# Kernel optimization log

Hardware: AMD Instinct MI355X
Metric: run time of the kernel (lower is better)

## Reference

```python
import jax, jax.numpy as jnp
import numpy as np

B, S, D, H = 4, 2048, 1024, 16
DK = D // H


def setup_inputs() -> dict:
    key = jax.random.key(0)
    k1, k2, k3, k4 = jax.random.split(key, 4)
    x = jax.random.normal(k1, (B, S, D), dtype=jnp.float32)
    # torch nn.Linear stores weight as [out, in]; y = x @ W.T + b
    w_qkv = jax.random.normal(k2, (3 * D, D), dtype=jnp.float32) * (1.0 / np.sqrt(D))
    b_qkv = jax.random.normal(k3, (3 * D,), dtype=jnp.float32) * 0.02
    w_o = jax.random.normal(k4, (D, D), dtype=jnp.float32) * (1.0 / np.sqrt(D))
    # causal mask: True where attention is disallowed (masked_fill semantics)
    mask = jnp.triu(jnp.ones((S, S), dtype=bool), k=1)[None, None]  # [1,1,S,S]
    return {"encodings_for_qkv": x, "mask": mask, "w_qkv": w_qkv, "b_qkv": b_qkv, "w_o": w_o}


def reference(encodings_for_qkv, mask, w_qkv, b_qkv, w_o):
    x = encodings_for_qkv
    qkv = x @ w_qkv.T + b_qkv                      # [B,S,3D]
    q, k, v = jnp.split(qkv, 3, axis=-1)           # each [B,S,D]

    def heads(t):
        return t.reshape(B, S, H, DK).transpose(0, 2, 1, 3)  # [B,H,S,DK]

    q, k, v = heads(q), heads(k), heads(v)
    scale = 1.0 / np.sqrt(DK).astype(np.float32)
    sims = jnp.einsum('bhqd,bhkd->bhqk', q, k) * scale       # [B,H,S,S]
    sims = jnp.where(mask, jnp.float32(-1e9), sims)
    attn = jax.nn.softmax(sims, axis=-1)
    out = jnp.einsum('bhqk,bhkd->bhqd', attn, v)             # [B,H,S,DK]
    out = out.transpose(0, 2, 1, 3).reshape(B, S, D)
    return out @ w_o.T
```

## Files before the change

### kernel.cpp

```cpp
#include <hip/hip_runtime.h>
#include <hip/hip_bf16.h>

typedef __attribute__((ext_vector_type(8))) __bf16 bf16x8;
typedef __attribute__((ext_vector_type(4))) __bf16 bf16x4;
typedef __attribute__((ext_vector_type(4))) float f32x4;

constexpr int B = 4, S = 2048, D = 1024, H = 16, DK = 64;

#define GLOAD16(gp, lp)                                                              \
  __builtin_amdgcn_global_load_lds((const __attribute__((address_space(1))) void*)(gp), \
                                   (__attribute__((address_space(3))) void*)(lp), 16, 0, 0)

__global__ __launch_bounds__(256) void convert_bf16(const float* __restrict__ X,
                                                    const float* __restrict__ Wqkv,
                                                    const float* __restrict__ Wo,
                                                    __bf16* __restrict__ Xb,
                                                    __bf16* __restrict__ Wqkvb,
                                                    __bf16* __restrict__ Wob) {
  const int NX = B * S * D;
  const int NW = 3 * D * D;
  const int NO = D * D;
  const int total8 = (NX + NW + NO) / 8;
  for (int i = blockIdx.x * blockDim.x + threadIdx.x; i < total8;
       i += gridDim.x * blockDim.x) {
    const int e = i * 8;
    const float* src;
    __bf16* dst;
    int off;
    if (e < NX) {
      src = X; dst = Xb; off = e;
    } else if (e < NX + NW) {
      src = Wqkv; dst = Wqkvb; off = e - NX;
    } else {
      src = Wo; dst = Wob; off = e - NX - NW;
    }
    float4 a = *reinterpret_cast<const float4*>(src + off);
    float4 b = *reinterpret_cast<const float4*>(src + off + 4);
    bf16x8 v = {(__bf16)a.x, (__bf16)a.y, (__bf16)a.z, (__bf16)a.w,
                (__bf16)b.x, (__bf16)b.y, (__bf16)b.z, (__bf16)b.w};
    *reinterpret_cast<bf16x8*>(dst + off) = v;
  }
}

__global__ __launch_bounds__(256) void qkv_gemm(const __bf16* __restrict__ Xb,
                                                const __bf16* __restrict__ Wb,
                                                const float* __restrict__ bias,
                                                __bf16* __restrict__ Qb,
                                                __bf16* __restrict__ Kb,
                                                __bf16* __restrict__ VTb) {
  __shared__ __bf16 As[2][128 * 64];
  __shared__ __bf16 Bs[2][128 * 64];
  const int tid = threadIdx.x;
  const int lane = tid & 63;
  const int w = tid >> 6;
  const int wr = w >> 1, wc = w & 1;
  const int lr = lane & 15, lb = lane >> 4;
  const int m0 = blockIdx.x * 128, n0 = blockIdx.y * 128;

  int srow[4], sgcol[4];
#pragma unroll
  for (int rnd = 0; rnd < 4; ++rnd) {
    const int i = rnd * 256 + tid;
    srow[rnd] = i >> 3;
    sgcol[rnd] = ((i & 7) ^ (srow[rnd] & 7)) << 3;
  }

  f32x4 acc[4][4];
#pragma unroll
  for (int i = 0; i < 4; ++i)
#pragma unroll
    for (int j = 0; j < 4; ++j) acc[i][j] = f32x4{0.f, 0.f, 0.f, 0.f};

#pragma unroll
  for (int rnd = 0; rnd < 4; ++rnd) {
    GLOAD16(&Xb[(size_t)(m0 + srow[rnd]) * D + sgcol[rnd]],
            (char*)&As[0][0] + rnd * 4096 + w * 1024);
    GLOAD16(&Wb[(size_t)(n0 + srow[rnd]) * D + sgcol[rnd]],
            (char*)&Bs[0][0] + rnd * 4096 + w * 1024);
  }
  __syncthreads();

  int cur = 0;
  for (int k0 = 0; k0 < D; k0 += 64) {
    if (k0 + 64 < D) {
#pragma unroll
      for (int rnd = 0; rnd < 4; ++rnd) {
        GLOAD16(&Xb[(size_t)(m0 + srow[rnd]) * D + k0 + 64 + sgcol[rnd]],
                (char*)&As[cur ^ 1][0] + rnd * 4096 + w * 1024);
        GLOAD16(&Wb[(size_t)(n0 + srow[rnd]) * D + k0 + 64 + sgcol[rnd]],
                (char*)&Bs[cur ^ 1][0] + rnd * 4096 + w * 1024);
      }
    }

    bf16x8 af[4][2], bfr[4][2];
#pragma unroll
    for (int m = 0; m < 4; ++m) {
      const int row = wr * 64 + m * 16 + lr;
#pragma unroll
      for (int ks = 0; ks < 2; ++ks)
        af[m][ks] = *reinterpret_cast<const bf16x8*>(
            (const char*)&As[cur][0] + row * 128 + (((ks * 32 + lb * 8) << 1) ^ ((row & 7) << 4)));
    }
#pragma unroll
    for (int n = 0; n < 4; ++n) {
      const int row = wc * 64 + n * 16 + lr;
#pragma unroll
      for (int ks = 0; ks < 2; ++ks)
        bfr[n][ks] = *reinterpret_cast<const bf16x8*>(
            (const char*)&Bs[cur][0] + row * 128 + (((ks * 32 + lb * 8) << 1) ^ ((row & 7) << 4)));
    }
#pragma unroll
    for (int m = 0; m < 4; ++m)
#pragma unroll
      for (int n = 0; n < 4; ++n) {
        acc[m][n] = __builtin_amdgcn_mfma_f32_16x16x32_bf16(af[m][0], bfr[n][0], acc[m][n], 0, 0, 0);
        acc[m][n] = __builtin_amdgcn_mfma_f32_16x16x32_bf16(af[m][1], bfr[n][1], acc[m][n], 0, 0, 0);
      }
    __syncthreads();
    cur ^= 1;
  }

  const int seg = n0 >> 10;
  if (seg == 2) {
#pragma unroll
    for (int m = 0; m < 4; ++m) {
      const int tb = m0 + wr * 64 + m * 16 + lb * 4;
      const int bb2 = tb >> 11;
      const int s = tb & 2047;
#pragma unroll
      for (int n = 0; n < 4; ++n) {
        const int c = n0 + wc * 64 + n * 16 + lr;
        const int cc = c & 1023;
        const int h = cc >> 6, dk = cc & 63;
        const float bv = bias[c];
        bf16x4 pv;
#pragma unroll
        for (int r = 0; r < 4; ++r) pv[r] = (__bf16)(acc[m][n][r] + bv);
        *reinterpret_cast<bf16x4*>(
            &VTb[(((size_t)bb2 * H + h) * DK + dk) * S + s]) = pv;
      }
    }
  } else {
#pragma unroll
    for (int m = 0; m < 4; ++m)
#pragma unroll
      for (int n = 0; n < 4; ++n) {
        const int c = n0 + wc * 64 + n * 16 + lr;
        const int cc = c & 1023;
        const int h = cc >> 6, dk = cc & 63;
        const float bv = bias[c];
#pragma unroll
        for (int r = 0; r < 4; ++r) {
          const int t = m0 + wr * 64 + m * 16 + lb * 4 + r;
          const int bb2 = t >> 11;
          const int s = t & 2047;
          const float v = acc[m][n][r] + bv;
          const size_t bh = (size_t)bb2 * H + h;
          if (seg == 0)
            Qb[(bh * S + s) * DK + dk] = (__bf16)(v * 0.180336893f);
          else
            Kb[(bh * S + s) * DK + dk] = (__bf16)v;
        }
      }
  }
}

__global__ __launch_bounds__(512, 4) void attn_fwd(const __bf16* __restrict__ Qb,
                                                   const __bf16* __restrict__ Kb,
                                                   const __bf16* __restrict__ VTb,
                                                   __bf16* __restrict__ AO) {
  __shared__ __bf16 Kl[2][64 * 64];
  __shared__ __bf16 Vl[2][64 * 64];
  __shared__ __bf16 Ps[8][16][72];
  const int tid = threadIdx.x;
  const int lane = tid & 63;
  const int w = tid >> 6;
  const int lr = lane & 15, lb = lane >> 4;

  const int flat = blockIdx.x;
  const int xcd = flat & 7;
  const int idx = flat >> 3;
  const int hg = idx & 7;
  const int pr = idx >> 3;
  const int bh = hg * 8 + xcd;
  const int bb = bh >> 4, h = bh & 15;

  const __bf16* Q = Qb + (size_t)bh * S * DK;
  const __bf16* K = Kb + (size_t)bh * S * DK;
  const __bf16* VT = VTb + (size_t)bh * DK * S;

  const int srow = tid >> 3;
  const int sc8 = (tid & 7) * 8;
  const int sbyte = srow * 128 + sc8 * 2;
  const int sswz = (srow & 7) << 4;
  const int rsw = (lr & 7) << 4;

  bf16x8 ones;
#pragma unroll
  for (int i = 0; i < 8; ++i) ones[i] = (__bf16)1.0f;

  for (int pass = 0; pass < 2; ++pass) {
    const int qt = pass ? (15 - pr) : pr;
    const int q0w = qt * 128 + w * 16;
    const int nt = 2 * qt + 2;
    const int ntw = 2 * qt + 1 + (w >> 2);

    bf16x8 qf[2];
#pragma unroll
    for (int d = 0; d < 2; ++d)
      qf[d] = *reinterpret_cast<const bf16x8*>(
          &Q[(size_t)(q0w + lr) * DK + d * 32 + lb * 8]);

    {
      bf16x8 k0 = *reinterpret_cast<const bf16x8*>(K + (size_t)srow * DK + sc8);
      bf16x8 v0 = *reinterpret_cast<const bf16x8*>(VT + (size_t)srow * S + sc8);
      *reinterpret_cast<bf16x8*>((char*)&Kl[0][0] + (sbyte ^ sswz)) = k0;
      *reinterpret_cast<bf16x8*>((char*)&Vl[0][0] + (sbyte ^ sswz)) = v0;
    }
    __syncthreads();

    f32x4 o[4], lsum;
#pragma unroll
    for (int n = 0; n < 4; ++n) o[n] = f32x4{0.f, 0.f, 0.f, 0.f};
    lsum = f32x4{0.f, 0.f, 0.f, 0.f};
    float mrun = -1e30f;

    int cur = 0;
    for (int t = 0; t < nt; ++t) {
      const int kv0 = t * 64;
      const bool have_next = (t + 1 < nt);
      bf16x8 gk0, gv0;
      if (have_next) {
        gk0 = *reinterpret_cast<const bf16x8*>(K + ((size_t)(kv0 + 64) + srow) * DK + sc8);
        gv0 = *reinterpret_cast<const bf16x8*>(VT + (size_t)srow * S + (kv0 + 64) + sc8);
      }

      if (t < ntw) {
        const char* kbase = (const char*)&Kl[cur][0];
        const char* vbase = (const char*)&Vl[cur][0];
        bf16x8 kf[4][2];
#pragma unroll
        for (int kc = 0; kc < 4; ++kc) {
          const int row = kc * 16 + lr;
#pragma unroll
          for (int d = 0; d < 2; ++d)
            kf[kc][d] = *reinterpret_cast<const bf16x8*>(
                kbase + row * 128 + ((d * 64 + lb * 16) ^ rsw));
        }

        f32x4 st[4];
        __builtin_amdgcn_s_setprio(1);
#pragma unroll
        for (int kc = 0; kc < 4; ++kc) {
          f32x4 z = f32x4{0.f, 0.f, 0.f, 0.f};
          z = __builtin_amdgcn_mfma_f32_16x16x32_bf16(kf[kc][0], qf[0], z, 0, 0, 0);
          z = __builtin_amdgcn_mfma_f32_16x16x32_bf16(kf[kc][1], qf[1], z, 0, 0, 0);
          st[kc] = z;
        }
        __builtin_amdgcn_s_setprio(0);

        if (t == ntw - 1) {
          const int qg = q0w + lr;
#pragma unroll
          for (int kc = 0; kc < 4; ++kc)
#pragma unroll
            for (int r = 0; r < 4; ++r) {
              const int kg = kv0 + kc * 16 + 4 * lb + r;
              if (kg > qg) st[kc][r] = -1e30f;
            }
        }

        float a0 = fmaxf(fmaxf(st[0][0], st[0][1]), fmaxf(st[0][2], st[0][3]));
        float a1 = fmaxf(fmaxf(st[1][0], st[1][1]), fmaxf(st[1][2], st[1][3]));
        float a2 = fmaxf(fmaxf(st[2][0], st[2][1]), fmaxf(st[2][2], st[2][3]));
        float a3 = fmaxf(fmaxf(st[3][0], st[3][1]), fmaxf(st[3][2], st[3][3]));
        float mx = fmaxf(fmaxf(a0, a1), fmaxf(a2, a3));
        mx = fmaxf(mx, __shfl_xor(mx, 16, 64));
        mx = fmaxf(mx, __shfl_xor(mx, 32, 64));

        if (__any(mx > mrun + 11.f)) {
          const float nm = fmaxf(mrun, mx);
          const float alpha = exp2f(mrun - nm);
          mrun = nm;
#pragma unroll
          for (int r = 0; r < 4; ++r) {
            const float ao = __shfl(alpha, 4 * lb + r, 64);
#pragma unroll
            for (int n = 0; n < 4; ++n) o[n][r] *= ao;
            lsum[r] *= ao;
          }
        }

#pragma unroll
        for (int kc = 0; kc < 4; ++kc) {
          bf16x4 pk;
#pragma unroll
          for (int r = 0; r < 4; ++r) pk[r] = (__bf16)exp2f(st[kc][r] - mrun);
          *reinterpret_cast<bf16x4*>(&Ps[w][lr][kc * 16 + 4 * lb]) = pk;
        }

        asm volatile("s_waitcnt lgkmcnt(0)" ::: "memory");
        __builtin_amdgcn_sched_barrier(0);

        bf16x8 pa[2];
#pragma unroll
        for (int ks = 0; ks < 2; ++ks)
          pa[ks] = *reinterpret_cast<const bf16x8*>(&Ps[w][lr][ks * 32 + lb * 8]);
        bf16x8 vf[4][2];
#pragma unroll
        for (int n = 0; n < 4; ++n) {
          const int row = n * 16 + lr;
#pragma unroll
          for (int ks = 0; ks < 2; ++ks)
            vf[n][ks] = *reinterpret_cast<const bf16x8*>(
                vbase + row * 128 + ((ks * 64 + lb * 16) ^ rsw));
        }

        __builtin_amdgcn_s_setprio(1);
#pragma unroll
        for (int n = 0; n < 4; ++n) {
          o[n] = __builtin_amdgcn_mfma_f32_16x16x32_bf16(pa[0], vf[n][0], o[n], 0, 0, 0);
          o[n] = __builtin_amdgcn_mfma_f32_16x16x32_bf16(pa[1], vf[n][1], o[n], 0, 0, 0);
        }
        lsum = __builtin_amdgcn_mfma_f32_16x16x32_bf16(pa[0], ones, lsum, 0, 0, 0);
        lsum = __builtin_amdgcn_mfma_f32_16x16x32_bf16(pa[1], ones, lsum, 0, 0, 0);
        __builtin_amdgcn_s_setprio(0);
      }

      if (have_next) {
        *reinterpret_cast<bf16x8*>((char*)&Kl[cur ^ 1][0] + (sbyte ^ sswz)) = gk0;
        *reinterpret_cast<bf16x8*>((char*)&Vl[cur ^ 1][0] + (sbyte ^ sswz)) = gv0;
      }
      __syncthreads();
      cur ^= 1;
    }

#pragma unroll
    for (int r = 0; r < 4; ++r) {
      const float inv = 1.f / lsum[r];
      const int q = q0w + 4 * lb + r;
#pragma unroll
      for (int n = 0; n < 4; ++n)
        AO[((size_t)(bb * S + q)) * D + h * DK + n * 16 + lr] = (__bf16)(o[n][r] * inv);
    }
  }
}

__global__ __launch_bounds__(256) void out_gemm(const __bf16* __restrict__ AOp,
                                                const __bf16* __restrict__ Wb,
                                                float* __restrict__ Out) {
  __shared__ __bf16 As[2][128 * 64];
  __shared__ __bf16 Bs[2][128 * 64];
  const int tid = threadIdx.x;
  const int lane = tid & 63;
  const int w = tid >> 6;
  const int wr = w >> 1, wc = w & 1;
  const int lr = lane & 15, lb = lane >> 4;
  const int m0 = blockIdx.x * 128, n0 = blockIdx.y * 128;

  int srow[4], sgcol[4];
#pragma unroll
  for (int rnd = 0; rnd < 4; ++rnd) {
    const int i = rnd * 256 + tid;
    srow[rnd] = i >> 3;
    sgcol[rnd] = ((i & 7) ^ (srow[rnd] & 7)) << 3;
  }

  f32x4 acc[4][4];
#pragma unroll
  for (int i = 0; i < 4; ++i)
#pragma unroll
    for (int j = 0; j < 4; ++j) acc[i][j] = f32x4{0.f, 0.f, 0.f, 0.f};

#pragma unroll
  for (int rnd = 0; rnd < 4; ++rnd) {
    GLOAD16(&AOp[(size_t)(m0 + srow[rnd]) * D + sgcol[rnd]],
            (char*)&As[0][0] + rnd * 4096 + w * 1024);
    GLOAD16(&Wb[(size_t)(n0 + srow[rnd]) * D + sgcol[rnd]],
            (char*)&Bs[0][0] + rnd * 4096 + w * 1024);
  }
  __syncthreads();

  int cur = 0;
  for (int k0 = 0; k0 < D; k0 += 64) {
    if (k0 + 64 < D) {
#pragma unroll
      for (int rnd = 0; rnd < 4; ++rnd) {
        GLOAD16(&AOp[(size_t)(m0 + srow[rnd]) * D + k0 + 64 + sgcol[rnd]],
                (char*)&As[cur ^ 1][0] + rnd * 4096 + w * 1024);
        GLOAD16(&Wb[(size_t)(n0 + srow[rnd]) * D + k0 + 64 + sgcol[rnd]],
                (char*)&Bs[cur ^ 1][0] + rnd * 4096 + w * 1024);
      }
    }

    bf16x8 af[4][2], bfr[4][2];
#pragma unroll
    for (int m = 0; m < 4; ++m) {
      const int row = wr * 64 + m * 16 + lr;
#pragma unroll
      for (int ks = 0; ks < 2; ++ks)
        af[m][ks] = *reinterpret_cast<const bf16x8*>(
            (const char*)&As[cur][0] + row * 128 + (((ks * 32 + lb * 8) << 1) ^ ((row & 7) << 4)));
    }
#pragma unroll
    for (int n = 0; n < 4; ++n) {
      const int row = wc * 64 + n * 16 + lr;
#pragma unroll
      for (int ks = 0; ks < 2; ++ks)
        bfr[n][ks] = *reinterpret_cast<const bf16x8*>(
            (const char*)&Bs[cur][0] + row * 128 + (((ks * 32 + lb * 8) << 1) ^ ((row & 7) << 4)));
    }
#pragma unroll
    for (int m = 0; m < 4; ++m)
#pragma unroll
      for (int n = 0; n < 4; ++n) {
        acc[m][n] = __builtin_amdgcn_mfma_f32_16x16x32_bf16(af[m][0], bfr[n][0], acc[m][n], 0, 0, 0);
        acc[m][n] = __builtin_amdgcn_mfma_f32_16x16x32_bf16(af[m][1], bfr[n][1], acc[m][n], 0, 0, 0);
      }
    __syncthreads();
    cur ^= 1;
  }

#pragma unroll
  for (int m = 0; m < 4; ++m)
#pragma unroll
    for (int n = 0; n < 4; ++n)
#pragma unroll
      for (int r = 0; r < 4; ++r)
        Out[(size_t)(m0 + wr * 64 + m * 16 + lb * 4 + r) * D + n0 + wc * 64 + n * 16 + lr] =
            acc[m][n][r];
}

extern "C" void kernel_launch(void* const* d_in, const int* in_sizes, int n_in,
                              void* d_out, int out_size, void* d_ws, size_t ws_size,
                              hipStream_t stream) {
  (void)in_sizes; (void)n_in; (void)out_size; (void)ws_size;
  const float* x = (const float*)d_in[0];
  const float* w_qkv = (const float*)d_in[2];
  const float* b_qkv = (const float*)d_in[3];
  const float* w_o = (const float*)d_in[4];
  float* out = (float*)d_out;

  const size_t qkv_elems = (size_t)B * H * S * DK;
  __bf16* Qb = (__bf16*)d_ws;
  __bf16* Kb = Qb + qkv_elems;
  __bf16* VTb = Kb + qkv_elems;
  __bf16* AO = VTb + qkv_elems;
  __bf16* Xb = AO + qkv_elems;
  __bf16* Wqkvb = Xb + (size_t)B * S * D;
  __bf16* Wob = Wqkvb + (size_t)3 * D * D;

  convert_bf16<<<2048, 256, 0, stream>>>(x, w_qkv, w_o, Xb, Wqkvb, Wob);
  qkv_gemm<<<dim3(64, 24), 256, 0, stream>>>(Xb, Wqkvb, b_qkv, Qb, Kb, VTb);
  attn_fwd<<<dim3(8 * (B * H)), 512, 0, stream>>>(Qb, Kb, VTb, AO);
  out_gemm<<<dim3(64, 8), 256, 0, stream>>>(AO, Wob, out);
}
```

Measured before the change: 166.7 us.

## Process two query tiles per attention block sharing each loaded K/V tile

The attention kernel previously ran two sequential passes per block (query tiles pr and 15-pr), each streaming its own K/V range. It now processes query tiles pr and pr+8 concurrently in one KV loop, so each K/V tile loaded into shared memory and the K/V fragments read from it serve both query tiles. This roughly halves K/V global and LDS traffic for the overlapping range, at the cost of doubled accumulator registers and a second P buffer in shared memory. The block-to-tile mapping is also reworked to balance the causal workload across blocks.

```diff
diff --git a/kernel.cpp b/kernel.cpp
--- a/kernel.cpp
+++ b/kernel.cpp
@@ -171,7 +171,8 @@
                                                    __bf16* __restrict__ AO) {
   __shared__ __bf16 Kl[2][64 * 64];
   __shared__ __bf16 Vl[2][64 * 64];
-  __shared__ __bf16 Ps[8][16][72];
+  __shared__ __bf16 PsA[8][16][72];
+  __shared__ __bf16 PsB[8][16][72];
   const int tid = threadIdx.x;
   const int lane = tid & 63;
   const int w = tid >> 6;
@@ -179,15 +180,22 @@
 
   const int flat = blockIdx.x;
   const int xcd = flat & 7;
-  const int idx = flat >> 3;
-  const int hg = idx & 7;
-  const int pr = idx >> 3;
+  const int hg = (flat >> 3) & 7;
+  const int s = flat >> 6;
+  const int pr = (s < 4) ? s : (11 - s);
   const int bh = hg * 8 + xcd;
   const int bb = bh >> 4, h = bh & 15;
 
+  const int qtA = pr, qtB = pr + 8;
   const __bf16* Q = Qb + (size_t)bh * S * DK;
   const __bf16* K = Kb + (size_t)bh * S * DK;
   const __bf16* VT = VTb + (size_t)bh * DK * S;
+
+  const int q0A = qtA * 128 + w * 16;
+  const int q0B = qtB * 128 + w * 16;
+  const int ntwA = 2 * qtA + 1 + (w >> 2);
+  const int ntwB = 2 * qtB + 1 + (w >> 2);
+  const int nt = 2 * qtB + 2;
 
   const int srow = tid >> 3;
   const int sc8 = (tid & 7) * 8;
@@ -199,68 +207,69 @@
 #pragma unroll
   for (int i = 0; i < 8; ++i) ones[i] = (__bf16)1.0f;
 
-  for (int pass = 0; pass < 2; ++pass) {
-    const int qt = pass ? (15 - pr) : pr;
-    const int q0w = qt * 128 + w * 16;
-    const int nt = 2 * qt + 2;
-    const int ntw = 2 * qt + 1 + (w >> 2);
-
-    bf16x8 qf[2];
-#pragma unroll
-    for (int d = 0; d < 2; ++d)
-      qf[d] = *reinterpret_cast<const bf16x8*>(
-          &Q[(size_t)(q0w + lr) * DK + d * 32 + lb * 8]);
-
-    {
-      bf16x8 k0 = *reinterpret_cast<const bf16x8*>(K + (size_t)srow * DK + sc8);
-      bf16x8 v0 = *reinterpret_cast<const bf16x8*>(VT + (size_t)srow * S + sc8);
-      *reinterpret_cast<bf16x8*>((char*)&Kl[0][0] + (sbyte ^ sswz)) = k0;
-      *reinterpret_cast<bf16x8*>((char*)&Vl[0][0] + (sbyte ^ sswz)) = v0;
-    }
-    __syncthreads();
-
-    f32x4 o[4], lsum;
-#pragma unroll
-    for (int n = 0; n < 4; ++n) o[n] = f32x4{0.f, 0.f, 0.f, 0.f};
-    lsum = f32x4{0.f, 0.f, 0.f, 0.f};
-    float mrun = -1e30f;
-
-    int cur = 0;
-    for (int t = 0; t < nt; ++t) {
-      const int kv0 = t * 64;
-      const bool have_next = (t + 1 < nt);
-      bf16x8 gk0, gv0;
-      if (have_next) {
-        gk0 = *reinterpret_cast<const bf16x8*>(K + ((size_t)(kv0 + 64) + srow) * DK + sc8);
-        gv0 = *reinterpret_cast<const bf16x8*>(VT + (size_t)srow * S + (kv0 + 64) + sc8);
-      }
-
-      if (t < ntw) {
-        const char* kbase = (const char*)&Kl[cur][0];
-        const char* vbase = (const char*)&Vl[cur][0];
-        bf16x8 kf[4][2];
-#pragma unroll
-        for (int kc = 0; kc < 4; ++kc) {
-          const int row = kc * 16 + lr;
-#pragma unroll
-          for (int d = 0; d < 2; ++d)
-            kf[kc][d] = *reinterpret_cast<const bf16x8*>(
-                kbase + row * 128 + ((d * 64 + lb * 16) ^ rsw));
-        }
-
+  bf16x8 qfA[2], qfB[2];
+#pragma unroll
+  for (int d = 0; d < 2; ++d) {
+    qfA[d] = *reinterpret_cast<const bf16x8*>(&Q[(size_t)(q0A + lr) * DK + d * 32 + lb * 8]);
+    qfB[d] = *reinterpret_cast<const bf16x8*>(&Q[(size_t)(q0B + lr) * DK + d * 32 + lb * 8]);
+  }
+
+  {
+    bf16x8 k0 = *reinterpret_cast<const bf16x8*>(K + (size_t)srow * DK + sc8);
+    bf16x8 v0 = *reinterpret_cast<const bf16x8*>(VT + (size_t)srow * S + sc8);
+    *reinterpret_cast<bf16x8*>((char*)&Kl[0][0] + (sbyte ^ sswz)) = k0;
+    *reinterpret_cast<bf16x8*>((char*)&Vl[0][0] + (sbyte ^ sswz)) = v0;
+  }
+  __syncthreads();
+
+  f32x4 oA[4], oB[4], lsA, lsB;
+#pragma unroll
+  for (int n = 0; n < 4; ++n) {
+    oA[n] = f32x4{0.f, 0.f, 0.f, 0.f};
+    oB[n] = f32x4{0.f, 0.f, 0.f, 0.f};
+  }
+  lsA = f32x4{0.f, 0.f, 0.f, 0.f};
+  lsB = f32x4{0.f, 0.f, 0.f, 0.f};
+  float mA = -1e30f, mB = -1e30f;
+
+  int cur = 0;
+  for (int t = 0; t < nt; ++t) {
+    const int kv0 = t * 64;
+    const bool have_next = (t + 1 < nt);
+    bf16x8 gk0, gv0;
+    if (have_next) {
+      gk0 = *reinterpret_cast<const bf16x8*>(K + ((size_t)(kv0 + 64) + srow) * DK + sc8);
+      gv0 = *reinterpret_cast<const bf16x8*>(VT + (size_t)srow * S + (kv0 + 64) + sc8);
+    }
+
+    const bool actA = (t < ntwA);
+    const bool actB = (t < ntwB);
+
+    if (actB) {
+      const char* kbase = (const char*)&Kl[cur][0];
+      bf16x8 kf[4][2];
+#pragma unroll
+      for (int kc = 0; kc < 4; ++kc) {
+        const int row = kc * 16 + lr;
+#pragma unroll
+        for (int d = 0; d < 2; ++d)
+          kf[kc][d] = *reinterpret_cast<const bf16x8*>(
+              kbase + row * 128 + ((d * 64 + lb * 16) ^ rsw));
+      }
+
+      {
         f32x4 st[4];
         __builtin_amdgcn_s_setprio(1);
 #pragma unroll
         for (int kc = 0; kc < 4; ++kc) {
           f32x4 z = f32x4{0.f, 0.f, 0.f, 0.f};
-          z = __builtin_amdgcn_mfma_f32_16x16x32_bf16(kf[kc][0], qf[0], z, 0, 0, 0);
-          z = __builtin_amdgcn_mfma_f32_16x16x32_bf16(kf[kc][1], qf[1], z, 0, 0, 0);
+          z = __builtin_amdgcn_mfma_f32_16x16x32_bf16(kf[kc][0], qfB[0], z, 0, 0, 0);
+          z = __builtin_amdgcn_mfma_f32_16x16x32_bf16(kf[kc][1], qfB[1], z, 0, 0, 0);
           st[kc] = z;
         }
         __builtin_amdgcn_s_setprio(0);
-
-        if (t == ntw - 1) {
-          const int qg = q0w + lr;
+        if (t == ntwB - 1) {
+          const int qg = q0B + lr;
 #pragma unroll
           for (int kc = 0; kc < 4; ++kc)
 #pragma unroll
@@ -269,7 +278,6 @@
               if (kg > qg) st[kc][r] = -1e30f;
             }
         }
-
         float a0 = fmaxf(fmaxf(st[0][0], st[0][1]), fmaxf(st[0][2], st[0][3]));
         float a1 = fmaxf(fmaxf(st[1][0], st[1][1]), fmaxf(st[1][2], st[1][3]));
         float a2 = fmaxf(fmaxf(st[2][0], st[2][1]), fmaxf(st[2][2], st[2][3]));
@@ -277,72 +285,129 @@
         float mx = fmaxf(fmaxf(a0, a1), fmaxf(a2, a3));
         mx = fmaxf(mx, __shfl_xor(mx, 16, 64));
         mx = fmaxf(mx, __shfl_xor(mx, 32, 64));
-
-        if (__any(mx > mrun + 11.f)) {
-          const float nm = fmaxf(mrun, mx);
-          const float alpha = exp2f(mrun - nm);
-          mrun = nm;
+        if (__any(mx > mB + 11.f)) {
+          const float nm = fmaxf(mB, mx);
+          const float alpha = exp2f(mB - nm);
+          mB = nm;
 #pragma unroll
           for (int r = 0; r < 4; ++r) {
             const float ao = __shfl(alpha, 4 * lb + r, 64);
 #pragma unroll
-            for (int n = 0; n < 4; ++n) o[n][r] *= ao;
-            lsum[r] *= ao;
+            for (int n = 0; n < 4; ++n) oB[n][r] *= ao;
+            lsB[r] *= ao;
           }
         }
-
 #pragma unroll
         for (int kc = 0; kc < 4; ++kc) {
           bf16x4 pk;
 #pragma unroll
-          for (int r = 0; r < 4; ++r) pk[r] = (__bf16)exp2f(st[kc][r] - mrun);
-          *reinterpret_cast<bf16x4*>(&Ps[w][lr][kc * 16 + 4 * lb]) = pk;
-        }
-
-        asm volatile("s_waitcnt lgkmcnt(0)" ::: "memory");
-        __builtin_amdgcn_sched_barrier(0);
-
-        bf16x8 pa[2];
-#pragma unroll
-        for (int ks = 0; ks < 2; ++ks)
-          pa[ks] = *reinterpret_cast<const bf16x8*>(&Ps[w][lr][ks * 32 + lb * 8]);
-        bf16x8 vf[4][2];
+          for (int r = 0; r < 4; ++r) pk[r] = (__bf16)exp2f(st[kc][r] - mB);
+          *reinterpret_cast<bf16x4*>(&PsB[w][lr][kc * 16 + 4 * lb]) = pk;
+        }
+      }
+
+      if (actA) {
+        f32x4 st[4];
+        __builtin_amdgcn_s_setprio(1);
+#pragma unroll
+        for (int kc = 0; kc < 4; ++kc) {
+          f32x4 z = f32x4{0.f, 0.f, 0.f, 0.f};
+          z = __builtin_amdgcn_mfma_f32_16x16x32_bf16(kf[kc][0], qfA[0], z, 0, 0, 0);
+          z = __builtin_amdgcn_mfma_f32_16x16x32_bf16(kf[kc][1], qfA[1], z, 0, 0, 0);
+          st[kc] = z;
+        }
+        __builtin_amdgcn_s_setprio(0);
+        if (t == ntwA - 1) {
+          const int qg = q0A + lr;
+#pragma unroll
+          for (int kc = 0; kc < 4; ++kc)
+#pragma unroll
+            for (int r = 0; r < 4; ++r) {
+              const int kg = kv0 + kc * 16 + 4 * lb + r;
+              if (kg > qg) st[kc][r] = -1e30f;
+            }
+        }
+        float a0 = fmaxf(fmaxf(st[0][0], st[0][1]), fmaxf(st[0][2], st[0][3]));
+        float a1 = fmaxf(fmaxf(st[1][0], st[1][1]), fmaxf(st[1][2], st[1][3]));
+        float a2 = fmaxf(fmaxf(st[2][0], st[2][1]), fmaxf(st[2][2], st[2][3]));
+        float a3 = fmaxf(fmaxf(st[3][0], st[3][1]), fmaxf(st[3][2], st[3][3]));
+        float mx = fmaxf(fmaxf(a0, a1), fmaxf(a2, a3));
+        mx = fmaxf(mx, __shfl_xor(mx, 16, 64));
+        mx = fmaxf(mx, __shfl_xor(mx, 32, 64));
+        if (__any(mx > mA + 11.f)) {
+          const float nm = fmaxf(mA, mx);
+          const float alpha = exp2f(mA - nm);
+          mA = nm;
+#pragma unroll
+          for (int r = 0; r < 4; ++r) {
+            const float ao = __shfl(alpha, 4 * lb + r, 64);
+#pragma unroll
+            for (int n = 0; n < 4; ++n) oA[n][r] *= ao;
+            lsA[r] *= ao;
+          }
+        }
+#pragma unroll
+        for (int kc = 0; kc < 4; ++kc) {
+          bf16x4 pk;
+#pragma unroll
+          for (int r = 0; r < 4; ++r) pk[r] = (__bf16)exp2f(st[kc][r] - mA);
+          *reinterpret_cast<bf16x4*>(&PsA[w][lr][kc * 16 + 4 * lb]) = pk;
+        }
+      }
+
+      asm volatile("s_waitcnt lgkmcnt(0)" ::: "memory");
+      __builtin_amdgcn_sched_barrier(0);
+
+      const char* vbase = (const char*)&Vl[cur][0];
+      __builtin_amdgcn_s_setprio(1);
+#pragma unroll
+      for (int ks = 0; ks < 2; ++ks) {
+        bf16x8 vf[4];
 #pragma unroll
         for (int n = 0; n < 4; ++n) {
           const int row = n * 16 + lr;
-#pragma unroll
-          for (int ks = 0; ks < 2; ++ks)
-            vf[n][ks] = *reinterpret_cast<const bf16x8*>(
-                vbase + row * 128 + ((ks * 64 + lb * 16) ^ rsw));
-        }
-
-        __builtin_amdgcn_s_setprio(1);
-#pragma unroll
-        for (int n = 0; n < 4; ++n) {
-          o[n] = __builtin_amdgcn_mfma_f32_16x16x32_bf16(pa[0], vf[n][0], o[n], 0, 0, 0);
-          o[n] = __builtin_amdgcn_mfma_f32_16x16x32_bf16(pa[1], vf[n][1], o[n], 0, 0, 0);
-        }
-        lsum = __builtin_amdgcn_mfma_f32_16x16x32_bf16(pa[0], ones, lsum, 0, 0, 0);
-        lsum = __builtin_amdgcn_mfma_f32_16x16x32_bf16(pa[1], ones, lsum, 0, 0, 0);
-        __builtin_amdgcn_s_setprio(0);
-      }
-
-      if (have_next) {
-        *reinterpret_cast<bf16x8*>((char*)&Kl[cur ^ 1][0] + (sbyte ^ sswz)) = gk0;
-        *reinterpret_cast<bf16x8*>((char*)&Vl[cur ^ 1][0] + (sbyte ^ sswz)) = gv0;
-      }
-      __syncthreads();
-      cur ^= 1;
-    }
-
-#pragma unroll
-    for (int r = 0; r < 4; ++r) {
-      const float inv = 1.f / lsum[r];
-      const int q = q0w + 4 * lb + r;
-#pragma unroll
-      for (int n = 0; n < 4; ++n)
-        AO[((size_t)(bb * S + q)) * D + h * DK + n * 16 + lr] = (__bf16)(o[n][r] * inv);
-    }
+          vf[n] = *reinterpret_cast<const bf16x8*>(
+              vbase + row * 128 + ((ks * 64 + lb * 16) ^ rsw));
+        }
+        bf16x8 paB = *reinterpret_cast<const bf16x8*>(&PsB[w][lr][ks * 32 + lb * 8]);
+#pragma unroll
+        for (int n = 0; n < 4; ++n)
+          oB[n] = __builtin_amdgcn_mfma_f32_16x16x32_bf16(paB, vf[n], oB[n], 0, 0, 0);
+        lsB = __builtin_amdgcn_mfma_f32_16x16x32_bf16(paB, ones, lsB, 0, 0, 0);
+        if (actA) {
+          bf16x8 paA = *reinterpret_cast<const bf16x8*>(&PsA[w][lr][ks * 32 + lb * 8]);
+#pragma unroll
+          for (int n = 0; n < 4; ++n)
+            oA[n] = __builtin_amdgcn_mfma_f32_16x16x32_bf16(paA, vf[n], oA[n], 0, 0, 0);
+          lsA = __builtin_amdgcn_mfma_f32_16x16x32_bf16(paA, ones, lsA, 0, 0, 0);
+        }
+      }
+      __builtin_amdgcn_s_setprio(0);
+    }
+
+    if (have_next) {
+      *reinterpret_cast<bf16x8*>((char*)&Kl[cur ^ 1][0] + (sbyte ^ sswz)) = gk0;
+      *reinterpret_cast<bf16x8*>((char*)&Vl[cur ^ 1][0] + (sbyte ^ sswz)) = gv0;
+    }
+    __syncthreads();
+    cur ^= 1;
+  }
+
+#pragma unroll
+  for (int r = 0; r < 4; ++r) {
+    const float invA = 1.f / lsA[r];
+    const int qA = q0A + 4 * lb + r;
+#pragma unroll
+    for (int n = 0; n < 4; ++n)
+      AO[((size_t)(bb * S + qA)) * D + h * DK + n * 16 + lr] = (__bf16)(oA[n][r] * invA);
+  }
+#pragma unroll
+  for (int r = 0; r < 4; ++r) {
+    const float invB = 1.f / lsB[r];
+    const int qB = q0B + 4 * lb + r;
+#pragma unroll
+    for (int n = 0; n < 4; ++n)
+      AO[((size_t)(bb * S + qB)) * D + h * DK + n * 16 + lr] = (__bf16)(oB[n][r] * invB);
   }
 }
 
```

New measurement: 195.8 us. 1.17x slower.
